# Performance work log

Measured on AMD Instinct MI355X. Metric: run time of the kernel, lower is better.

The kernel has to match this reference:

```python
import jax, jax.numpy as jnp
import numpy as np

N_NODES = 50000
N_EDGES = 800000
IN_DIM = 128
HID = 128
TIME = 6.0
STEPS = 12


def setup_inputs() -> dict:
    key = jax.random.key(0)
    ks = jax.random.split(key, 8)
    gat_out = jax.random.normal(ks[0], (N_NODES, IN_DIM), dtype=jnp.float32)
    edge_index = jax.random.randint(ks[1], (2, N_EDGES), 0, N_NODES, dtype=jnp.int64)
    # scale weights like PyTorch Linear default (uniform-ish magnitude)
    W_in = jax.random.normal(ks[2], (IN_DIM, HID), dtype=jnp.float32) * (1.0 / np.sqrt(IN_DIM))
    b_in = jnp.zeros((HID,), dtype=jnp.float32)
    W1 = jax.random.normal(ks[3], (HID, 2 * HID), dtype=jnp.float32) * (1.0 / np.sqrt(HID))
    b1 = jnp.zeros((2 * HID,), dtype=jnp.float32)
    W2 = jax.random.normal(ks[4], (2 * HID, HID), dtype=jnp.float32) * (1.0 / np.sqrt(2 * HID))
    b2 = jnp.zeros((HID,), dtype=jnp.float32)
    clearance = jnp.full((1,), 0.1, dtype=jnp.float32)
    return {"gat_out": gat_out, "edge_index": edge_index, "W_in": W_in, "b_in": b_in,
            "W1": W1, "b1": b1, "W2": W2, "b2": b2, "clearance": clearance}


def reference(gat_out, edge_index, W_in, b_in, W1, b1, W2, b2, clearance):
    N = gat_out.shape[0]
    dt = TIME / STEPS
    src, dst = edge_index[0], edge_index[1]
    h = jnp.tanh(gat_out @ W_in + b_in)  # [N, HID]
    # degree is identical each Euler step in the original; hoist it once
    deg = jax.ops.segment_sum(jnp.ones((src.shape[0],), dtype=h.dtype), dst, num_segments=N)
    deg = jnp.clip(deg, 1.0, None)[:, None]  # [N, 1]
    decay = jax.nn.relu(clearance)  # [1]

    def step(h, _):
        agg = jax.ops.segment_sum(h[src], dst, num_segments=N) / deg  # [N, HID]
        diff = jnp.tanh(jax.nn.gelu(agg @ W1 + b1, approximate=False) @ W2 + b2)
        h = h + (diff - decay * h) * dt
        return h, None

    h, _ = jax.lax.scan(step, h, None, length=STEPS)
    return h
```

## Files before the change

### kernel.cpp

```cpp
#include <hip/hip_runtime.h>
#include <math.h>

#define N_NODES 50000
#define N_EDGES 800000
#define HID 128
#define H2 256
#define STEPS 12
#define DT 0.5f

#define SCAN_B 256
#define NB ((N_NODES + SCAN_B - 1) / SCAN_B)
#define NODE_BLOCKS ((N_NODES + 31) / 32)
#define N_PAD (NODE_BLOCKS * 32)
#define CSR_CAP (N_EDGES + 8 * N_NODES)

typedef __attribute__((ext_vector_type(8))) short bf16x8;
typedef __attribute__((ext_vector_type(4))) float f32x4;

__device__ inline unsigned short f2bf(float x) {
    unsigned int u = __float_as_uint(x);
    unsigned int r = (u + 0x7FFFu + ((u >> 16) & 1u)) >> 16;
    return (unsigned short)r;
}
__device__ inline float bf2f(unsigned short b) {
    return __uint_as_float(((unsigned int)b) << 16);
}
__device__ inline float u2f(unsigned int u) { return __uint_as_float(u); }

__device__ inline float fast_tanh(float x) {
    float xc = fminf(fmaxf(x, -9.0f), 9.0f);
    float t = __builtin_amdgcn_exp2f(xc * 2.8853900817779268f);
    return 1.0f - 2.0f * __builtin_amdgcn_rcpf(t + 1.0f);
}

__device__ inline float fast_gelu(float x) {
    float u  = x * 0.70710678118654752f;
    float au = fabsf(u);
    float t  = __builtin_amdgcn_rcpf(fmaf(0.3275911f, au, 1.0f));
    float poly = t * (0.254829592f + t * (-0.284496736f + t * (1.421413741f +
                 t * (-1.453152027f + t * 1.061405429f))));
    float ex = __builtin_amdgcn_exp2f(-au * au * 1.4426950408889634f);
    float erfv = copysignf(1.0f - poly * ex, u);
    return 0.5f * x * (1.0f + erfv);
}


__global__ void k_init(int* __restrict__ counts, int* __restrict__ csr,
                       unsigned short* __restrict__ a, unsigned short* __restrict__ b) {
    int i = blockIdx.x * 256 + threadIdx.x;
    if (i < N_NODES) counts[i] = 0;
    if (i < CSR_CAP) csr[i] = N_NODES;
    if (i < (N_PAD - N_NODES) * HID) {
        a[(size_t)N_NODES * HID + i] = 0;
        b[(size_t)N_NODES * HID + i] = 0;
    }
}

__global__ void k_hist(const int* __restrict__ dst, int* __restrict__ counts) {
    int e = blockIdx.x * 256 + threadIdx.x;
    if (e < N_EDGES) atomicAdd(&counts[dst[e]], 1);
}

__global__ void k_blocksum(const int* __restrict__ counts, int* __restrict__ bsum) {
    __shared__ int s[SCAN_B];
    int idx = blockIdx.x * SCAN_B + threadIdx.x;
    int v = (idx < N_NODES) ? ((counts[idx] + 7) & ~7) : 0;
    s[threadIdx.x] = v;
    __syncthreads();
    for (int off = SCAN_B / 2; off > 0; off >>= 1) {
        if (threadIdx.x < off) s[threadIdx.x] += s[threadIdx.x + off];
        __syncthreads();
    }
    if (threadIdx.x == 0) bsum[blockIdx.x] = s[0];
}

__global__ void k_scan_bsums(int* __restrict__ bsum, int* __restrict__ offsets) {
    __shared__ int s[SCAN_B];
    int tid = threadIdx.x;
    int v = (tid < NB) ? bsum[tid] : 0;
    s[tid] = v;
    __syncthreads();
    for (int off = 1; off < SCAN_B; off <<= 1) {
        int t = 0;
        if (tid >= off) t = s[tid - off];
        __syncthreads();
        s[tid] += t;
        __syncthreads();
    }
    if (tid < NB) bsum[tid] = s[tid] - v;
    if (tid == SCAN_B - 1) offsets[N_NODES] = s[SCAN_B - 1];
}

__global__ void k_offsets(const int* __restrict__ counts, const int* __restrict__ bsum,
                          int* __restrict__ offsets, int* __restrict__ cursor) {
    __shared__ int s[SCAN_B];
    int idx = blockIdx.x * SCAN_B + threadIdx.x;
    int v = (idx < N_NODES) ? ((counts[idx] + 7) & ~7) : 0;
    s[threadIdx.x] = v;
    __syncthreads();
    for (int off = 1; off < SCAN_B; off <<= 1) {
        int t = 0;
        if ((int)threadIdx.x >= off) t = s[threadIdx.x - off];
        __syncthreads();
        s[threadIdx.x] += t;
        __syncthreads();
    }
    if (idx < N_NODES) {
        int excl = s[threadIdx.x] - v;
        int o = bsum[blockIdx.x] + excl;
        offsets[idx] = o;
        cursor[idx]  = o;
    }
}

__global__ void k_scatter(const int* __restrict__ src, const int* __restrict__ dst,
                          int* __restrict__ cursor, int* __restrict__ csr_src) {
    int e = blockIdx.x * 256 + threadIdx.x;
    if (e < N_EDGES) {
        int d = dst[e];
        int p = atomicAdd(&cursor[d], 1);
        csr_src[p] = src[e];
    }
}


__global__ void k_pack(const float* __restrict__ W, int K, int N,
                       unsigned short* __restrict__ hi, unsigned short* __restrict__ lo) {
    int KT = K >> 5, NT = N >> 4;
    int t = blockIdx.x * 256 + threadIdx.x;
    if (t >= KT * NT * 64) return;
    int l = t & 63, tile = t >> 6;
    int kt = tile % KT, nt = tile / KT;
    int n  = nt * 16 + (l & 15);
    int k0 = kt * 32 + (l >> 4) * 8;
    int base = ((nt * KT + kt) * 64 + l) * 8;
    for (int j = 0; j < 8; j++) {
        float w = W[(size_t)(k0 + j) * N + n];
        unsigned short h = f2bf(w);
        hi[base + j] = h;
        lo[base + j] = f2bf(w - bf2f(h));
    }
}


__global__ __launch_bounds__(256, 3) void k_h0_mfma(
    const float* __restrict__ gat,
    const unsigned short* __restrict__ wh, const unsigned short* __restrict__ wl,
    const float* __restrict__ b_in, float* __restrict__ h,
    unsigned short* __restrict__ hbf) {
    __shared__ unsigned short Ahi[32][136];
    __shared__ unsigned short Alo[32][136];
    int tid = threadIdx.x;
    int node0 = blockIdx.x * 32;

    for (int idx = tid; idx < 32 * 64; idx += 256) {
        int m = idx >> 6, c = (idx & 63) * 2;
        float2 v;
        if (node0 + m < N_NODES) v = *(const float2*)&gat[(size_t)(node0 + m) * 128 + c];
        else { v.x = 0.f; v.y = 0.f; }
        unsigned short h0 = f2bf(v.x), h1 = f2bf(v.y);
        unsigned short l0 = f2bf(v.x - bf2f(h0)), l1 = f2bf(v.y - bf2f(h1));
        *(unsigned int*)&Ahi[m][c] = (unsigned int)h0 | ((unsigned int)h1 << 16);
        *(unsigned int*)&Alo[m][c] = (unsigned int)l0 | ((unsigned int)l1 << 16);
    }
    __syncthreads();

    int l = tid & 63, wv = tid >> 6;
    int c15 = l & 15, q = l >> 4;
    f32x4 acc[2][2] = {};
#pragma unroll
    for (int kt = 0; kt < 4; kt++) {
        bf16x8 ah[2], al[2];
#pragma unroll
        for (int mt = 0; mt < 2; mt++) {
            ah[mt] = *(const bf16x8*)&Ahi[mt * 16 + c15][kt * 32 + q * 8];
            al[mt] = *(const bf16x8*)&Alo[mt * 16 + c15][kt * 32 + q * 8];
        }
#pragma unroll
        for (int nn = 0; nn < 2; nn++) {
            int nt = wv * 2 + nn;
            bf16x8 bh = *(const bf16x8*)&wh[(size_t)((nt * 4 + kt) * 64 + l) * 8];
            bf16x8 bl = *(const bf16x8*)&wl[(size_t)((nt * 4 + kt) * 64 + l) * 8];
#pragma unroll
            for (int mt = 0; mt < 2; mt++) {
                acc[mt][nn] = __builtin_amdgcn_mfma_f32_16x16x32_bf16(ah[mt], bh, acc[mt][nn], 0, 0, 0);
                acc[mt][nn] = __builtin_amdgcn_mfma_f32_16x16x32_bf16(ah[mt], bl, acc[mt][nn], 0, 0, 0);
                acc[mt][nn] = __builtin_amdgcn_mfma_f32_16x16x32_bf16(al[mt], bh, acc[mt][nn], 0, 0, 0);
            }
        }
    }
#pragma unroll
    for (int nn = 0; nn < 2; nn++) {
        int col = (wv * 2 + nn) * 16 + c15;
        float bb = b_in[col];
#pragma unroll
        for (int mt = 0; mt < 2; mt++)
#pragma unroll
            for (int r = 0; r < 4; r++) {
                int node = node0 + mt * 16 + q * 4 + r;
                if (node < N_NODES) {
                    float v = fast_tanh(acc[mt][nn][r] + bb);
                    h[(size_t)node * 128 + col]   = v;
                    hbf[(size_t)node * 128 + col] = f2bf(v);
                }
            }
    }
}


#define ACC8(V) \
    a0 += u2f((V).x << 16); a1 += u2f((V).x & 0xFFFF0000u); \
    a2 += u2f((V).y << 16); a3 += u2f((V).y & 0xFFFF0000u); \
    a4 += u2f((V).z << 16); a5 += u2f((V).z & 0xFFFF0000u); \
    a6 += u2f((V).w << 16); a7 += u2f((V).w & 0xFFFF0000u);

__global__ __launch_bounds__(512, 4) void k_step(
    const unsigned short* __restrict__ hbf_in,
    float* __restrict__ h, unsigned short* __restrict__ hbf_out,
    const int* __restrict__ offsets, const int* __restrict__ csr,
    const int* __restrict__ cnt,
    const unsigned short* __restrict__ w1h, const unsigned short* __restrict__ w1l,
    const float* __restrict__ b1,
    const unsigned short* __restrict__ w2h, const unsigned short* __restrict__ w2l,
    const float* __restrict__ b2, const float* __restrict__ clr) {
    __shared__ unsigned short Ahi[32][136];
    __shared__ unsigned short Alo[32][136];
    __shared__ unsigned short Y[32][264];
    int tid = threadIdx.x, l = tid & 63, wv = tid >> 6;
    int c15 = l & 15, q = l >> 4;
    int node0 = blockIdx.x * 32;
    int g  = l >> 4;
    int cl = l & 15;

    {
        int m = wv * 4 + g;
        int node = node0 + m;
        float a0 = 0.f, a1 = 0.f, a2 = 0.f, a3 = 0.f;
        float a4 = 0.f, a5 = 0.f, a6 = 0.f, a7 = 0.f;
        int deg = 0;
        if (node < N_NODES) {
            deg = cnt[node];
            int beg = offsets[node];
            int end = beg + ((deg + 7) & ~7);
            const unsigned short* hb = hbf_in + cl * 8;
            if (beg < end) {
                int4 i0 = *(const int4*)&csr[beg];
                int4 i1 = *(const int4*)&csr[beg + 4];
                for (int e = beg; e < end; e += 8) {
                    int enx = (e + 8 < end) ? (e + 8) : e;
                    int4 j0 = *(const int4*)&csr[enx];
                    int4 j1 = *(const int4*)&csr[enx + 4];
                    uint4 w0 = *(const uint4*)&hb[((unsigned)i0.x) << 7];
                    uint4 w1 = *(const uint4*)&hb[((unsigned)i0.y) << 7];
                    uint4 w2 = *(const uint4*)&hb[((unsigned)i0.z) << 7];
                    uint4 w3 = *(const uint4*)&hb[((unsigned)i0.w) << 7];
                    uint4 w4 = *(const uint4*)&hb[((unsigned)i1.x) << 7];
                    uint4 w5 = *(const uint4*)&hb[((unsigned)i1.y) << 7];
                    uint4 w6 = *(const uint4*)&hb[((unsigned)i1.z) << 7];
                    uint4 w7 = *(const uint4*)&hb[((unsigned)i1.w) << 7];
                    i0 = j0; i1 = j1;
                    ACC8(w0); ACC8(w1); ACC8(w2); ACC8(w3);
                    ACC8(w4); ACC8(w5); ACC8(w6); ACC8(w7);
                }
            }
        }
        float inv = (deg > 1) ? 1.0f / (float)deg : 1.0f;
        float x0 = a0 * inv, x1 = a1 * inv, x2 = a2 * inv, x3 = a3 * inv;
        float x4 = a4 * inv, x5 = a5 * inv, x6 = a6 * inv, x7 = a7 * inv;
        unsigned short h0 = f2bf(x0), h1 = f2bf(x1), h2 = f2bf(x2), h3 = f2bf(x3);
        unsigned short h4 = f2bf(x4), h5 = f2bf(x5), h6 = f2bf(x6), h7 = f2bf(x7);
        uint4 ohi;
        ohi.x = (unsigned int)h0 | ((unsigned int)h1 << 16);
        ohi.y = (unsigned int)h2 | ((unsigned int)h3 << 16);
        ohi.z = (unsigned int)h4 | ((unsigned int)h5 << 16);
        ohi.w = (unsigned int)h6 | ((unsigned int)h7 << 16);
        *(uint4*)&Ahi[m][cl * 8] = ohi;
        unsigned short l0 = f2bf(x0 - bf2f(h0)), l1 = f2bf(x1 - bf2f(h1));
        unsigned short l2 = f2bf(x2 - bf2f(h2)), l3 = f2bf(x3 - bf2f(h3));
        unsigned short l4 = f2bf(x4 - bf2f(h4)), l5 = f2bf(x5 - bf2f(h5));
        unsigned short l6 = f2bf(x6 - bf2f(h6)), l7 = f2bf(x7 - bf2f(h7));
        uint4 olo;
        olo.x = (unsigned int)l0 | ((unsigned int)l1 << 16);
        olo.y = (unsigned int)l2 | ((unsigned int)l3 << 16);
        olo.z = (unsigned int)l4 | ((unsigned int)l5 << 16);
        olo.w = (unsigned int)l6 | ((unsigned int)l7 << 16);
        *(uint4*)&Alo[m][cl * 8] = olo;
    }
    __syncthreads();

    {
        f32x4 acc1[2][2] = {};
#pragma unroll
        for (int kt = 0; kt < 4; kt++) {
            bf16x8 ah[2], al[2];
#pragma unroll
            for (int mt = 0; mt < 2; mt++) {
                ah[mt] = *(const bf16x8*)&Ahi[mt * 16 + c15][kt * 32 + q * 8];
                al[mt] = *(const bf16x8*)&Alo[mt * 16 + c15][kt * 32 + q * 8];
            }
#pragma unroll
            for (int nn = 0; nn < 2; nn++) {
                int nt = wv * 2 + nn;
                bf16x8 bh = *(const bf16x8*)&w1h[(size_t)((nt * 4 + kt) * 64 + l) * 8];
                bf16x8 bl = *(const bf16x8*)&w1l[(size_t)((nt * 4 + kt) * 64 + l) * 8];
#pragma unroll
                for (int mt = 0; mt < 2; mt++) {
                    acc1[mt][nn] = __builtin_amdgcn_mfma_f32_16x16x32_bf16(ah[mt], bh, acc1[mt][nn], 0, 0, 0);
                    acc1[mt][nn] = __builtin_amdgcn_mfma_f32_16x16x32_bf16(ah[mt], bl, acc1[mt][nn], 0, 0, 0);
                    acc1[mt][nn] = __builtin_amdgcn_mfma_f32_16x16x32_bf16(al[mt], bh, acc1[mt][nn], 0, 0, 0);
                }
            }
        }
#pragma unroll
        for (int nn = 0; nn < 2; nn++) {
            int col = (wv * 2 + nn) * 16 + c15;
            float bb = b1[col];
#pragma unroll
            for (int mt = 0; mt < 2; mt++)
#pragma unroll
                for (int r = 0; r < 4; r++) {
                    int row = mt * 16 + q * 4 + r;
                    float x = acc1[mt][nn][r] + bb;
                    Y[row][col] = f2bf(fast_gelu(x));
                }
        }
    }
    __syncthreads();

    f32x4 acc2[2] = {};
#pragma unroll
    for (int kt = 0; kt < 8; kt++) {
        bf16x8 ya[2];
#pragma unroll
        for (int mt = 0; mt < 2; mt++)
            ya[mt] = *(const bf16x8*)&Y[mt * 16 + c15][kt * 32 + q * 8];
        bf16x8 bh = *(const bf16x8*)&w2h[(size_t)((wv * 8 + kt) * 64 + l) * 8];
        bf16x8 bl = *(const bf16x8*)&w2l[(size_t)((wv * 8 + kt) * 64 + l) * 8];
#pragma unroll
        for (int mt = 0; mt < 2; mt++) {
            acc2[mt] = __builtin_amdgcn_mfma_f32_16x16x32_bf16(ya[mt], bh, acc2[mt], 0, 0, 0);
            acc2[mt] = __builtin_amdgcn_mfma_f32_16x16x32_bf16(ya[mt], bl, acc2[mt], 0, 0, 0);
        }
    }
    float decay = fmaxf(clr[0], 0.0f);
    {
        int col = wv * 16 + c15;
        float bb = b2[col];
#pragma unroll
        for (int mt = 0; mt < 2; mt++)
#pragma unroll
            for (int r = 0; r < 4; r++) {
                int node = node0 + mt * 16 + q * 4 + r;
                if (node < N_NODES) {
                    float hv = h[(size_t)node * 128 + col];
                    float diff = fast_tanh(acc2[mt][r] + bb);
                    float nh = hv + (diff - decay * hv) * DT;
                    h[(size_t)node * 128 + col]       = nh;
                    hbf_out[(size_t)node * 128 + col] = f2bf(nh);
                }
            }
    }
}


extern "C" void kernel_launch(void* const* d_in, const int* in_sizes, int n_in,
                              void* d_out, int out_size, void* d_ws, size_t ws_size,
                              hipStream_t stream) {
    const float* gat   = (const float*)d_in[0];
    const int*   edges = (const int*)d_in[1];
    const float* W_in  = (const float*)d_in[2];
    const float* b_in  = (const float*)d_in[3];
    const float* W1    = (const float*)d_in[4];
    const float* b1    = (const float*)d_in[5];
    const float* W2    = (const float*)d_in[6];
    const float* b2    = (const float*)d_in[7];
    const float* clr   = (const float*)d_in[8];
    float* h = (float*)d_out;

    const int* src = edges;
    const int* dst = edges + N_EDGES;

    char* ws = (char*)d_ws;
    size_t off = 0;
    auto alloc = [&](size_t bytes) -> void* {
        off = (off + 255) & ~(size_t)255;
        void* p = ws + off;
        off += bytes;
        return p;
    };
    int*   counts  = (int*)alloc(sizeof(int) * N_NODES);
    int*   offsets = (int*)alloc(sizeof(int) * (N_NODES + 1));
    int*   cursor  = (int*)alloc(sizeof(int) * N_NODES);
    int*   bsum    = (int*)alloc(sizeof(int) * NB);
    int*   csr_src = (int*)alloc(sizeof(int) * CSR_CAP);
    unsigned short* hbfA = (unsigned short*)alloc(sizeof(short) * (size_t)N_PAD * HID);
    unsigned short* hbfB = (unsigned short*)alloc(sizeof(short) * (size_t)N_PAD * HID);
    unsigned short* w1h  = (unsigned short*)alloc(sizeof(short) * HID * H2);
    unsigned short* w1l  = (unsigned short*)alloc(sizeof(short) * HID * H2);
    unsigned short* w2h  = (unsigned short*)alloc(sizeof(short) * H2 * HID);
    unsigned short* w2l  = (unsigned short*)alloc(sizeof(short) * H2 * HID);
    unsigned short* winh = (unsigned short*)alloc(sizeof(short) * HID * HID);
    unsigned short* winl = (unsigned short*)alloc(sizeof(short) * HID * HID);

    k_pack<<<16, 256, 0, stream>>>(W1, 128, 256, w1h, w1l);
    k_pack<<<16, 256, 0, stream>>>(W2, 256, 128, w2h, w2l);
    k_pack<<<8, 256, 0, stream>>>(W_in, 128, 128, winh, winl);

    k_init<<<(CSR_CAP + 255) / 256, 256, 0, stream>>>(counts, csr_src, hbfA, hbfB);
    k_hist<<<(N_EDGES + 255) / 256, 256, 0, stream>>>(dst, counts);
    k_blocksum<<<NB, 256, 0, stream>>>(counts, bsum);
    k_scan_bsums<<<1, SCAN_B, 0, stream>>>(bsum, offsets);
    k_offsets<<<NB, 256, 0, stream>>>(counts, bsum, offsets, cursor);
    k_scatter<<<(N_EDGES + 255) / 256, 256, 0, stream>>>(src, dst, cursor, csr_src);

    k_h0_mfma<<<NODE_BLOCKS, 256, 0, stream>>>(gat, winh, winl, b_in, h, hbfA);

    for (int s = 0; s < STEPS; s++) {
        const unsigned short* in = (s & 1) ? hbfB : hbfA;
        unsigned short*      out = (s & 1) ? hbfA : hbfB;
        k_step<<<NODE_BLOCKS, 512, 0, stream>>>(in, h, out, offsets, csr_src, counts,
                                                w1h, w1l, b1, w2h, w2l, b2, clr);
    }
}
```

Baseline: 816.5 us.

## Fuse Euler steps into one persistent cooperative kernel with atomic tile scheduling

Replaces the twelve per-step launches with a single cooperative persistent kernel. Its blocks pull 32-node tiles from a per-step atomic counter and meet at a grid-wide barrier between steps. This targets launch overhead and tail imbalance from uneven node degrees, and launch bounds are raised to allow more resident blocks. The cost is a grid sync per step, an atomic per tile and possible register pressure from the tighter launch bounds, with a fallback to the old per-step launches if the cooperative launch fails.

```diff
diff --git a/kernel.cpp b/kernel.cpp
--- a/kernel.cpp
+++ b/kernel.cpp
@@ -1,5 +1,8 @@
 #include <hip/hip_runtime.h>
+#include <hip/hip_cooperative_groups.h>
 #include <math.h>
+
+namespace cg = cooperative_groups;
 
 #define N_NODES 50000
 #define N_EDGES 800000
@@ -46,8 +49,10 @@
 
 
 __global__ void k_init(int* __restrict__ counts, int* __restrict__ csr,
-                       unsigned short* __restrict__ a, unsigned short* __restrict__ b) {
+                       unsigned short* __restrict__ a, unsigned short* __restrict__ b,
+                       int* __restrict__ tick) {
     int i = blockIdx.x * 256 + threadIdx.x;
+    if (i < STEPS) tick[i] = 0;
     if (i < N_NODES) counts[i] = 0;
     if (i < CSR_CAP) csr[i] = N_NODES;
     if (i < (N_PAD - N_NODES) * HID) {
@@ -214,7 +219,8 @@
     a4 += u2f((V).z << 16); a5 += u2f((V).z & 0xFFFF0000u); \
     a6 += u2f((V).w << 16); a7 += u2f((V).w & 0xFFFF0000u);
 
-__global__ __launch_bounds__(512, 4) void k_step(
+__device__ __forceinline__ void step_tile(
+    int bid, int tid,
     const unsigned short* __restrict__ hbf_in,
     float* __restrict__ h, unsigned short* __restrict__ hbf_out,
     const int* __restrict__ offsets, const int* __restrict__ csr,
@@ -222,13 +228,11 @@
     const unsigned short* __restrict__ w1h, const unsigned short* __restrict__ w1l,
     const float* __restrict__ b1,
     const unsigned short* __restrict__ w2h, const unsigned short* __restrict__ w2l,
-    const float* __restrict__ b2, const float* __restrict__ clr) {
-    __shared__ unsigned short Ahi[32][136];
-    __shared__ unsigned short Alo[32][136];
-    __shared__ unsigned short Y[32][264];
-    int tid = threadIdx.x, l = tid & 63, wv = tid >> 6;
+    const float* __restrict__ b2, float decay,
+    unsigned short (*Ahi)[136], unsigned short (*Alo)[136], unsigned short (*Y)[264]) {
+    int l = tid & 63, wv = tid >> 6;
     int c15 = l & 15, q = l >> 4;
-    int node0 = blockIdx.x * 32;
+    int node0 = bid * 32;
     int g  = l >> 4;
     int cl = l & 15;
 
@@ -342,7 +346,6 @@
             acc2[mt] = __builtin_amdgcn_mfma_f32_16x16x32_bf16(ya[mt], bl, acc2[mt], 0, 0, 0);
         }
     }
-    float decay = fmaxf(clr[0], 0.0f);
     {
         int col = wv * 16 + c15;
         float bb = b2[col];
@@ -359,6 +362,59 @@
                     hbf_out[(size_t)node * 128 + col] = f2bf(nh);
                 }
             }
+    }
+}
+
+
+__global__ __launch_bounds__(512, 8) void k_step(
+    const unsigned short* __restrict__ hbf_in,
+    float* __restrict__ h, unsigned short* __restrict__ hbf_out,
+    const int* __restrict__ offsets, const int* __restrict__ csr,
+    const int* __restrict__ cnt,
+    const unsigned short* __restrict__ w1h, const unsigned short* __restrict__ w1l,
+    const float* __restrict__ b1,
+    const unsigned short* __restrict__ w2h, const unsigned short* __restrict__ w2l,
+    const float* __restrict__ b2, const float* __restrict__ clr) {
+    __shared__ unsigned short Ahi[32][136];
+    __shared__ unsigned short Alo[32][136];
+    __shared__ unsigned short Y[32][264];
+    float decay = fmaxf(clr[0], 0.0f);
+    step_tile(blockIdx.x, threadIdx.x, hbf_in, h, hbf_out, offsets, csr, cnt,
+              w1h, w1l, b1, w2h, w2l, b2, decay, Ahi, Alo, Y);
+}
+
+
+__global__ __launch_bounds__(512, 8) void k_steps(
+    unsigned short* __restrict__ hbfA, unsigned short* __restrict__ hbfB,
+    float* __restrict__ h,
+    const int* __restrict__ offsets, const int* __restrict__ csr,
+    const int* __restrict__ cnt,
+    const unsigned short* __restrict__ w1h, const unsigned short* __restrict__ w1l,
+    const float* __restrict__ b1,
+    const unsigned short* __restrict__ w2h, const unsigned short* __restrict__ w2l,
+    const float* __restrict__ b2, const float* __restrict__ clr,
+    int* __restrict__ tick) {
+    __shared__ unsigned short Ahi[32][136];
+    __shared__ unsigned short Alo[32][136];
+    __shared__ unsigned short Y[32][264];
+    __shared__ int sBid;
+    cg::grid_group grid = cg::this_grid();
+    float decay = fmaxf(clr[0], 0.0f);
+    int tid = threadIdx.x;
+
+    for (int s = 0; s < STEPS; s++) {
+        const unsigned short* hin  = (s & 1) ? hbfB : hbfA;
+        unsigned short*       hout = (s & 1) ? hbfA : hbfB;
+        for (;;) {
+            __syncthreads();
+            if (tid == 0) sBid = atomicAdd(&tick[s], 1);
+            __syncthreads();
+            int bid = sBid;
+            if (bid >= NODE_BLOCKS) break;
+            step_tile(bid, tid, hin, h, hout, offsets, csr, cnt,
+                      w1h, w1l, b1, w2h, w2l, b2, decay, Ahi, Alo, Y);
+        }
+        if (s != STEPS - 1) grid.sync();
     }
 }
 
@@ -392,6 +448,7 @@
     int*   offsets = (int*)alloc(sizeof(int) * (N_NODES + 1));
     int*   cursor  = (int*)alloc(sizeof(int) * N_NODES);
     int*   bsum    = (int*)alloc(sizeof(int) * NB);
+    int*   tick    = (int*)alloc(sizeof(int) * STEPS);
     int*   csr_src = (int*)alloc(sizeof(int) * CSR_CAP);
     unsigned short* hbfA = (unsigned short*)alloc(sizeof(short) * (size_t)N_PAD * HID);
     unsigned short* hbfB = (unsigned short*)alloc(sizeof(short) * (size_t)N_PAD * HID);
@@ -406,7 +463,7 @@
     k_pack<<<16, 256, 0, stream>>>(W2, 256, 128, w2h, w2l);
     k_pack<<<8, 256, 0, stream>>>(W_in, 128, 128, winh, winl);
 
-    k_init<<<(CSR_CAP + 255) / 256, 256, 0, stream>>>(counts, csr_src, hbfA, hbfB);
+    k_init<<<(CSR_CAP + 255) / 256, 256, 0, stream>>>(counts, csr_src, hbfA, hbfB, tick);
     k_hist<<<(N_EDGES + 255) / 256, 256, 0, stream>>>(dst, counts);
     k_blocksum<<<NB, 256, 0, stream>>>(counts, bsum);
     k_scan_bsums<<<1, SCAN_B, 0, stream>>>(bsum, offsets);
@@ -415,10 +472,22 @@
 
     k_h0_mfma<<<NODE_BLOCKS, 256, 0, stream>>>(gat, winh, winl, b_in, h, hbfA);
 
-    for (int s = 0; s < STEPS; s++) {
-        const unsigned short* in = (s & 1) ? hbfB : hbfA;
-        unsigned short*      out = (s & 1) ? hbfA : hbfB;
-        k_step<<<NODE_BLOCKS, 512, 0, stream>>>(in, h, out, offsets, csr_src, counts,
-                                                w1h, w1l, b1, w2h, w2l, b2, clr);
-    }
-}
+    int occ = 0;
+    (void)hipOccupancyMaxActiveBlocksPerMultiprocessor(&occ, k_steps, 512, 0);
+    if (occ < 1) occ = 1;
+    int grid = occ * 256;
+    if (grid > NODE_BLOCKS) grid = NODE_BLOCKS;
+
+    void* args[] = { &hbfA, &hbfB, &h, &offsets, &csr_src, &counts,
+                     &w1h, &w1l, &b1, &w2h, &w2l, &b2, &clr, &tick };
+    hipError_t err = hipLaunchCooperativeKernel((const void*)k_steps, dim3(grid), dim3(512),
+                                                args, 0, stream);
+    if (err != hipSuccess) {
+        for (int s = 0; s < STEPS; s++) {
+            const unsigned short* in = (s & 1) ? hbfB : hbfA;
+            unsigned short*      out = (s & 1) ? hbfA : hbfB;
+            k_step<<<NODE_BLOCKS, 512, 0, stream>>>(in, h, out, offsets, csr_src, counts,
+                                                    w1h, w1l, b1, w2h, w2l, b2, clr);
+        }
+    }
+}
```

Result: slower. 1.990 ms (+143.7%).
